# Kernel tuning notes

Hardware: AMD Instinct MI355X
Metric: run time of the kernel (lower is better)

## Reference

```python
import jax, jax.numpy as jnp
import numpy as np

B, C, N = 8, 512, 2048
C8 = C // 8


def setup_inputs() -> dict:
    key = jax.random.key(0)
    kx, kq, kk, kv, kg = jax.random.split(key, 5)
    return {
        "x": jax.random.normal(kx, (B, C, N), dtype=jnp.float32),
        "Wq": jax.random.normal(kq, (C8, C), dtype=jnp.float32) * (1.0 / np.sqrt(C)),
        "Wk": jax.random.normal(kk, (C8, C), dtype=jnp.float32) * (1.0 / np.sqrt(C)),
        "Wv": jax.random.normal(kv, (C, C), dtype=jnp.float32) * (1.0 / np.sqrt(C)),
        # torch init is gamma=0.0; use a small random value so the attention
        # branch contributes to the output.
        "gamma": jax.random.uniform(kg, (1,), dtype=jnp.float32),
    }


def reference(x, Wq, Wk, Wv, gamma):
    # 1x1 convs == per-position linear maps over channels
    f = jnp.einsum("oc,bcn->bon", Wq, x)   # [B, C/8, N]
    g = jnp.einsum("oc,bcn->bon", Wk, x)   # [B, C/8, N]
    h = jnp.einsum("oc,bcn->bon", Wv, x)   # [B, C,   N]
    # scores[b,n,m] = sum_c f[b,c,n] * g[b,c,m]  (unscaled, as in source)
    scores = jnp.einsum("bcn,bcm->bnm", f, g)  # [B, N, N]
    # softmax over dim=1 (the query-position axis) — atypical but faithful
    beta = jax.nn.softmax(scores, axis=1)
    # o = gamma * h @ beta + x
    o = gamma[0] * jnp.einsum("bcn,bnm->bcm", h, beta) + x
    return o
```

## Files before the change

kernel.cpp:

```cpp
#include <hip/hip_runtime.h>
#include <hip/hip_bf16.h>
#include <math.h>

#define NB 8
#define NC 512
#define NN 2048

typedef unsigned short u16;
typedef __attribute__((ext_vector_type(8))) short short8;
typedef __attribute__((ext_vector_type(4))) float f32x4;

__device__ __forceinline__ float bf16_to_f32(u16 v) {
  union { unsigned int u; float f; } c; c.u = ((unsigned int)v) << 16; return c.f;
}
__device__ __forceinline__ u16 f32_to_bf16(float f) {
  __hip_bfloat16 h = __float2bfloat16(f);
  union { __hip_bfloat16 h; u16 u; } c; c.h = h; return c.u;
}
__device__ __forceinline__ void split2(float v, unsigned short& hi, unsigned short& lo) {
  hi = f32_to_bf16(v);
  lo = f32_to_bf16(v - bf16_to_f32(hi));
}

__device__ __forceinline__ void gl_lds16(const void* g, void* l) {
  __builtin_amdgcn_global_load_lds(
      (const __attribute__((address_space(1))) unsigned int*)g,
      (__attribute__((address_space(3))) unsigned int*)l, 16, 0, 0);
}

__device__ __forceinline__ void stage128x32(const u16* __restrict__ src, size_t row_base,
                                            int selems, int k0, u16* lds, int tid) {
#pragma unroll
  for (int s = 0; s < 2; ++s) {
    int flat = s * 4096 + tid * 16;
    int row = flat >> 6;
    int kb  = flat & 63;
    const char* g = (const char*)(src + (row_base + row) * (size_t)selems + k0) + kb;
    u16* l = lds + s * 2048 + (tid & ~63) * 8;
    gl_lds16(g, l);
  }
}

__global__ __launch_bounds__(256)
void xsplit_kernel(const float* __restrict__ x,
                   const float* __restrict__ Wq, const float* __restrict__ Wk,
                   const float* __restrict__ Wv,
                   u16* __restrict__ xThi, u16* __restrict__ xTlo,
                   u16* __restrict__ Whi, u16* __restrict__ Wlo) {
  const int b = blockIdx.z, c0 = blockIdx.y * 64, n0 = blockIdx.x * 64;
  const int tid = threadIdx.x;

  int fid = blockIdx.x + 32 * (blockIdx.y + 8 * blockIdx.z);
  if (fid < 320) {
    int idx = (fid * 256 + tid) * 4;
    int r = idx >> 9, c = idx & 511;
    const float* src;
    if (r < 64)       src = Wq + (size_t)r * NC + c;
    else if (r < 128) src = Wk + (size_t)(r - 64) * NC + c;
    else              src = Wv + (size_t)(r - 128) * NC + c;
    float4 v = *(const float4*)src;
    ushort4 hi, lo;
    split2(v.x, hi.x, lo.x); split2(v.y, hi.y, lo.y);
    split2(v.z, hi.z, lo.z); split2(v.w, hi.w, lo.w);
    *(ushort4*)&Whi[idx] = hi;
    *(ushort4*)&Wlo[idx] = lo;
  }

  __shared__ float t[64][65];
  const int tx = tid & 15, ty = tid >> 4;
#pragma unroll
  for (int r = 0; r < 4; ++r) {
    int c = r * 16 + ty;
    float4 v = *(const float4*)&x[((size_t)b * NC + c0 + c) * NN + n0 + tx * 4];
    t[c][tx * 4 + 0] = v.x; t[c][tx * 4 + 1] = v.y;
    t[c][tx * 4 + 2] = v.z; t[c][tx * 4 + 3] = v.w;
  }
  __syncthreads();
#pragma unroll
  for (int r = 0; r < 4; ++r) {
    int n = r * 16 + ty;
    ushort4 hi, lo;
    split2(t[tx * 4 + 0][n], hi.x, lo.x);
    split2(t[tx * 4 + 1][n], hi.y, lo.y);
    split2(t[tx * 4 + 2][n], hi.z, lo.z);
    split2(t[tx * 4 + 3][n], hi.w, lo.w);
    size_t off = ((size_t)b * NN + n0 + n) * NC + c0 + tx * 4;
    *(ushort4*)&xThi[off] = hi;
    *(ushort4*)&xTlo[off] = lo;
  }
}

__global__ __launch_bounds__(256)
void proj_mfma_kernel(const u16* __restrict__ xThi, const u16* __restrict__ xTlo,
                      const u16* __restrict__ Whi, const u16* __restrict__ Wlo,
                      u16* __restrict__ fgThi, u16* __restrict__ fgTlo,
                      u16* __restrict__ hw) {
  const int b  = blockIdx.z;
  const int n0 = blockIdx.x * 128;
  const int r0 = blockIdx.y * 128;
  const bool fg = (r0 == 0);

  __shared__ u16 Wh[2][128 * 32], Wl[2][128 * 32], Xh[2][128 * 32], Xl[2][128 * 32];

  const int tid = threadIdx.x, wave = tid >> 6, lane = tid & 63;
  const int quad = lane >> 4, l16 = lane & 15;
  const int wa = (wave >> 1) * 64, wb = (wave & 1) * 64;
  const size_t xrow = (size_t)b * NN + n0;

  f32x4 acc[4][4];
#pragma unroll
  for (int i = 0; i < 4; ++i)
#pragma unroll
    for (int j = 0; j < 4; ++j) acc[i][j] = (f32x4){0.f, 0.f, 0.f, 0.f};

  stage128x32(Whi, r0, NC, 0, Wh[0], tid);
  stage128x32(xThi, xrow, NC, 0, Xh[0], tid);
  if (fg) {
    stage128x32(Wlo, r0, NC, 0, Wl[0], tid);
    stage128x32(xTlo, xrow, NC, 0, Xl[0], tid);
  }

  const int KIT = NC / 32;
  for (int ki = 0; ki < KIT; ++ki) {
    __syncthreads();
    if (ki + 1 < KIT) {
      const int nb = (ki + 1) & 1, k1 = (ki + 1) * 32;
      stage128x32(Whi, r0, NC, k1, Wh[nb], tid);
      stage128x32(xThi, xrow, NC, k1, Xh[nb], tid);
      if (fg) {
        stage128x32(Wlo, r0, NC, k1, Wl[nb], tid);
        stage128x32(xTlo, xrow, NC, k1, Xl[nb], tid);
      }
    }
    const int cur = ki & 1;

    if (fg) {
      short8 ah[4], al[4], bh[4], bl[4];
#pragma unroll
      for (int i = 0; i < 4; ++i) {
        ah[i] = *(short8*)&Wh[cur][(wa + i * 16 + l16) * 32 + quad * 8];
        al[i] = *(short8*)&Wl[cur][(wa + i * 16 + l16) * 32 + quad * 8];
      }
#pragma unroll
      for (int j = 0; j < 4; ++j) {
        bh[j] = *(short8*)&Xh[cur][(wb + j * 16 + l16) * 32 + quad * 8];
        bl[j] = *(short8*)&Xl[cur][(wb + j * 16 + l16) * 32 + quad * 8];
      }
#pragma unroll
      for (int i = 0; i < 4; ++i)
#pragma unroll
        for (int j = 0; j < 4; ++j) {
          acc[i][j] = __builtin_amdgcn_mfma_f32_16x16x32_bf16(ah[i], bh[j], acc[i][j], 0, 0, 0);
          acc[i][j] = __builtin_amdgcn_mfma_f32_16x16x32_bf16(ah[i], bl[j], acc[i][j], 0, 0, 0);
          acc[i][j] = __builtin_amdgcn_mfma_f32_16x16x32_bf16(al[i], bh[j], acc[i][j], 0, 0, 0);
        }
    } else {
      short8 ah[4], bh[4];
#pragma unroll
      for (int i = 0; i < 4; ++i)
        ah[i] = *(short8*)&Xh[cur][(wa + i * 16 + l16) * 32 + quad * 8];
#pragma unroll
      for (int j = 0; j < 4; ++j)
        bh[j] = *(short8*)&Wh[cur][(wb + j * 16 + l16) * 32 + quad * 8];
#pragma unroll
      for (int i = 0; i < 4; ++i)
#pragma unroll
        for (int j = 0; j < 4; ++j)
          acc[i][j] = __builtin_amdgcn_mfma_f32_16x16x32_bf16(ah[i], bh[j], acc[i][j], 0, 0, 0);
    }
  }

  if (fg) {
#pragma unroll
    for (int i = 0; i < 4; ++i)
#pragma unroll
      for (int j = 0; j < 4; ++j) {
        int rb = wa + i * 16 + quad * 4;
        int n  = n0 + wb + j * 16 + l16;
        ushort4 hi, lo;
        split2(acc[i][j][0], hi.x, lo.x); split2(acc[i][j][1], hi.y, lo.y);
        split2(acc[i][j][2], hi.z, lo.z); split2(acc[i][j][3], hi.w, lo.w);
        size_t off = ((size_t)b * NN + n) * 128 + rb;
        *(ushort4*)&fgThi[off] = hi;
        *(ushort4*)&fgTlo[off] = lo;
      }
  } else {
#pragma unroll
    for (int i = 0; i < 4; ++i)
#pragma unroll
      for (int j = 0; j < 4; ++j) {
        int nb = n0 + wa + i * 16 + quad * 4;
        int c  = r0 - 128 + wb + j * 16 + l16;
        ushort4 hi;
        hi.x = f32_to_bf16(acc[i][j][0]); hi.y = f32_to_bf16(acc[i][j][1]);
        hi.z = f32_to_bf16(acc[i][j][2]); hi.w = f32_to_bf16(acc[i][j][3]);
        *(ushort4*)&hw[((size_t)b * NC + c) * NN + nb] = hi;
      }
  }
}

__global__ __launch_bounds__(512, 4)
void attn_out_kernel(const u16* __restrict__ fgThi, const u16* __restrict__ fgTlo,
                     const u16* __restrict__ hw, const float* __restrict__ x,
                     const float* __restrict__ gamma, float* __restrict__ out) {
  const int s = blockIdx.x;
  const int xcd = s & 7;
  const int t = s >> 3;
  const int mt = t & 31;
  const int hi6 = t >> 5;
  const int combo = (hi6 << 3) | xcd;
  const int b = combo >> 1;
  const int ch = combo & 1;
  const int m0 = mt * 64;
  const int c0 = ch * 256;

  __shared__ u16 Fh[2][64 * 64], Fl[2][64 * 64];
  __shared__ u16 Hs[256 * 64];
  __shared__ u16 Ps[64 * 64];
  float* Dn = (float*)Ps;

  const int tid = threadIdx.x, wave = tid >> 6, lane = tid & 63;
  const int quad = lane >> 4, l16 = lane & 15;
  const int ws_n = (wave >> 2) * 32, ws_m = (wave & 3) * 16;
  const int wv_c = (wave >> 1) * 64, wv_m = (wave & 1) * 32;

  const size_t frow = (size_t)b * NN;
  const size_t hrow = (size_t)b * NC + c0;

  short8 gh[2], gl[2];
#pragma unroll
  for (int k = 0; k < 2; ++k) {
    size_t o = (frow + m0 + ws_m + l16) * 128 + 64 + k * 32 + quad * 8;
    gh[k] = *(const short8*)&fgThi[o];
    gl[k] = *(const short8*)&fgTlo[o];
  }

  {
    int flat = tid * 16;
    int row = flat >> 7, chunk = (flat >> 4) & 7;
    int kb = ((chunk ^ (row & 7)) << 4);
    gl_lds16((const char*)(fgThi + (frow + row) * 128) + kb, Fh[0] + (tid & ~63) * 8);
    gl_lds16((const char*)(fgTlo + (frow + row) * 128) + kb, Fl[0] + (tid & ~63) * 8);
#pragma unroll
    for (int s2 = 0; s2 < 4; ++s2) {
      int f2 = s2 * 8192 + tid * 16;
      int r2 = f2 >> 7, c2 = (f2 >> 4) & 7;
      gl_lds16((const char*)(hw + (hrow + r2) * NN) + ((c2 ^ (r2 & 7)) << 4),
               Hs + s2 * 4096 + (tid & ~63) * 8);
    }
  }
  __syncthreads();

  float dsum = 0.f;
  f32x4 ao[4][2];
#pragma unroll
  for (int i = 0; i < 4; ++i)
#pragma unroll
    for (int j = 0; j < 2; ++j) ao[i][j] = (f32x4){0.f, 0.f, 0.f, 0.f};

  const int NT = NN / 64;
  for (int it = 0; it < NT; ++it) {
    const int cur = it & 1;

    if (it > 0) {
      const int n1 = it * 64;
#pragma unroll
      for (int s2 = 0; s2 < 4; ++s2) {
        int f2 = s2 * 8192 + tid * 16;
        int r2 = f2 >> 7, c2 = (f2 >> 4) & 7;
        gl_lds16((const char*)(hw + (hrow + r2) * NN + n1) + ((c2 ^ (r2 & 7)) << 4),
                 Hs + s2 * 4096 + (tid & ~63) * 8);
      }
    }
    if (it + 1 < NT) {
      const int n1 = (it + 1) * 64;
      int flat = tid * 16;
      int row = flat >> 7, chunk = (flat >> 4) & 7;
      int kb = ((chunk ^ (row & 7)) << 4);
      gl_lds16((const char*)(fgThi + (frow + n1 + row) * 128) + kb,
               Fh[cur ^ 1] + (tid & ~63) * 8);
      gl_lds16((const char*)(fgTlo + (frow + n1 + row) * 128) + kb,
               Fl[cur ^ 1] + (tid & ~63) * 8);
    }

    f32x4 as[2];
#pragma unroll
    for (int i = 0; i < 2; ++i) as[i] = (f32x4){0.f, 0.f, 0.f, 0.f};
#pragma unroll
    for (int k = 0; k < 2; ++k) {
      short8 fh[2], fl[2];
#pragma unroll
      for (int i = 0; i < 2; ++i) {
        int rr = ws_n + i * 16 + l16;
        int ci = (((k * 4 + quad) ^ (rr & 7)) << 3);
        fh[i] = *(short8*)&Fh[cur][rr * 64 + ci];
        fl[i] = *(short8*)&Fl[cur][rr * 64 + ci];
      }
#pragma unroll
      for (int i = 0; i < 2; ++i) {
        as[i] = __builtin_amdgcn_mfma_f32_16x16x32_bf16(fh[i], gh[k], as[i], 0, 0, 0);
        as[i] = __builtin_amdgcn_mfma_f32_16x16x32_bf16(fh[i], gl[k], as[i], 0, 0, 0);
        as[i] = __builtin_amdgcn_mfma_f32_16x16x32_bf16(fl[i], gh[k], as[i], 0, 0, 0);
      }
    }

    {
      int m = ws_m + l16;
#pragma unroll
      for (int i = 0; i < 2; ++i) {
        float e0 = __expf(as[i][0]);
        float e1 = __expf(as[i][1]);
        float e2 = __expf(as[i][2]);
        float e3 = __expf(as[i][3]);
        dsum += (e0 + e1) + (e2 + e3);
        ushort4 pk;
        pk.x = f32_to_bf16(e0); pk.y = f32_to_bf16(e1);
        pk.z = f32_to_bf16(e2); pk.w = f32_to_bf16(e3);
        int nb = ws_n * 2 + i * 32 + quad * 8;
        int chunk = nb >> 4;
        int off = (nb & 15) >> 1;
        *(ushort4*)&Ps[m * 64 + ((chunk ^ (m & 7)) << 3) + off] = pk;
      }
    }

    if (it + 1 < NT) asm volatile("s_waitcnt vmcnt(2)" ::: "memory");
    else             asm volatile("s_waitcnt vmcnt(0)" ::: "memory");
    asm volatile("s_waitcnt lgkmcnt(0)" ::: "memory");
    __builtin_amdgcn_s_barrier();

#pragma unroll
    for (int k = 0; k < 2; ++k) {
      short8 hh[4], pb[2];
#pragma unroll
      for (int i = 0; i < 4; ++i) {
        int rr = wv_c + i * 16 + l16;
        hh[i] = *(short8*)&Hs[rr * 64 + ((((k * 4 + quad)) ^ (rr & 7)) << 3)];
      }
#pragma unroll
      for (int j = 0; j < 2; ++j) {
        int rm = wv_m + j * 16 + l16;
        pb[j] = *(short8*)&Ps[rm * 64 + ((((k * 4 + quad)) ^ (rm & 7)) << 3)];
      }
#pragma unroll
      for (int i = 0; i < 4; ++i)
#pragma unroll
        for (int j = 0; j < 2; ++j)
          ao[i][j] = __builtin_amdgcn_mfma_f32_16x16x32_bf16(hh[i], pb[j], ao[i][j], 0, 0, 0);
    }

    __syncthreads();
  }

  dsum += __shfl_xor(dsum, 16);
  dsum += __shfl_xor(dsum, 32);
  if (tid < 64) Dn[tid] = 0.f;
  __syncthreads();
  if (quad == 0) atomicAdd(&Dn[ws_m + l16], dsum);
  __syncthreads();

  const float g = gamma[0];
  float invd[2];
#pragma unroll
  for (int j = 0; j < 2; ++j)
    invd[j] = g / Dn[wv_m + j * 16 + l16];

#pragma unroll
  for (int i = 0; i < 4; ++i) {
#pragma unroll
    for (int j = 0; j < 2; ++j) {
      const int c = c0 + wv_c + i * 16 + quad * 4;
      const int m = m0 + wv_m + j * 16 + l16;
#pragma unroll
      for (int r = 0; r < 4; ++r) {
        size_t off = ((size_t)b * NC + c + r) * NN + m;
        out[off] = fmaf(invd[j], ao[i][j][r], x[off]);
      }
    }
  }
}

extern "C" void kernel_launch(void* const* d_in, const int* in_sizes, int n_in,
                              void* d_out, int out_size, void* d_ws, size_t ws_size,
                              hipStream_t stream) {
  const float* x     = (const float*)d_in[0];
  const float* Wq    = (const float*)d_in[1];
  const float* Wk    = (const float*)d_in[2];
  const float* Wv    = (const float*)d_in[3];
  const float* gamma = (const float*)d_in[4];
  float* out = (float*)d_out;

  char* ws = (char*)d_ws;
  u16*   xThi  = (u16*)ws;
  u16*   xTlo  = (u16*)(ws + 16777216);
  u16*   Whi   = (u16*)(ws + 33554432);
  u16*   Wlo   = (u16*)(ws + 34209792);
  u16*   fgThi = (u16*)(ws + 67108864);
  u16*   fgTlo = (u16*)(ws + 71303168);
  u16*   hw    = (u16*)(ws + 75497472);

  xsplit_kernel<<<dim3(NN / 64, NC / 64, NB), 256, 0, stream>>>(
      x, Wq, Wk, Wv, xThi, xTlo, Whi, Wlo);
  proj_mfma_kernel<<<dim3(NN / 128, 5, NB), 256, 0, stream>>>(
      xThi, xTlo, Whi, Wlo, fgThi, fgTlo, hw);
  attn_out_kernel<<<dim3(512), 512, 0, stream>>>(fgThi, fgTlo, hw, x, gamma, out);
}
```

Baseline: 199.2 us.

## Split projection into separate fg and h kernels; raise MFMA wave priority in attention

The combined projection kernel, where one block in five did the three-pass split-bf16 f/g work (a load imbalance), becomes two kernels. proj_fg uses 64-row tiles across two blocks per position tile, so the costly 3-MFMA work is spread over more blocks. proj_h handles the single-pass Wv projection with no divergent branches or unused lo-buffer LDS. In the attention kernel, s_setprio raises wave priority around the MFMA sections to favour matrix issue. The split adds an extra kernel launch and reloads the x tiles for the fg blocks.

```diff
diff --git a/kernel.cpp b/kernel.cpp
--- a/kernel.cpp
+++ b/kernel.cpp
@@ -39,6 +39,15 @@
     u16* l = lds + s * 2048 + (tid & ~63) * 8;
     gl_lds16(g, l);
   }
+}
+
+__device__ __forceinline__ void stage64x32(const u16* __restrict__ src, size_t row_base,
+                                           int selems, int k0, u16* lds, int tid) {
+  int flat = tid * 16;
+  int row = flat >> 6;
+  int kb  = flat & 63;
+  const char* g = (const char*)(src + (row_base + row) * (size_t)selems + k0) + kb;
+  gl_lds16(g, lds + (tid & ~63) * 8);
 }
 
 __global__ __launch_bounds__(256)
@@ -91,16 +100,87 @@
 }
 
 __global__ __launch_bounds__(256)
-void proj_mfma_kernel(const u16* __restrict__ xThi, const u16* __restrict__ xTlo,
-                      const u16* __restrict__ Whi, const u16* __restrict__ Wlo,
-                      u16* __restrict__ fgThi, u16* __restrict__ fgTlo,
-                      u16* __restrict__ hw) {
+void proj_fg_kernel(const u16* __restrict__ xThi, const u16* __restrict__ xTlo,
+                    const u16* __restrict__ Whi, const u16* __restrict__ Wlo,
+                    u16* __restrict__ fgThi, u16* __restrict__ fgTlo) {
   const int b  = blockIdx.z;
   const int n0 = blockIdx.x * 128;
-  const int r0 = blockIdx.y * 128;
-  const bool fg = (r0 == 0);
-
-  __shared__ u16 Wh[2][128 * 32], Wl[2][128 * 32], Xh[2][128 * 32], Xl[2][128 * 32];
+  const int r0 = blockIdx.y * 64;
+
+  __shared__ u16 Wh[2][64 * 32], Wl[2][64 * 32], Xh[2][128 * 32], Xl[2][128 * 32];
+
+  const int tid = threadIdx.x, wave = tid >> 6, lane = tid & 63;
+  const int quad = lane >> 4, l16 = lane & 15;
+  const int wa = (wave >> 1) * 32, wb = (wave & 1) * 64;
+  const size_t xrow = (size_t)b * NN + n0;
+
+  f32x4 acc[2][4];
+#pragma unroll
+  for (int i = 0; i < 2; ++i)
+#pragma unroll
+    for (int j = 0; j < 4; ++j) acc[i][j] = (f32x4){0.f, 0.f, 0.f, 0.f};
+
+  stage64x32(Whi, r0, NC, 0, Wh[0], tid);
+  stage64x32(Wlo, r0, NC, 0, Wl[0], tid);
+  stage128x32(xThi, xrow, NC, 0, Xh[0], tid);
+  stage128x32(xTlo, xrow, NC, 0, Xl[0], tid);
+
+  const int KIT = NC / 32;
+  for (int ki = 0; ki < KIT; ++ki) {
+    __syncthreads();
+    if (ki + 1 < KIT) {
+      const int nb = (ki + 1) & 1, k1 = (ki + 1) * 32;
+      stage64x32(Whi, r0, NC, k1, Wh[nb], tid);
+      stage64x32(Wlo, r0, NC, k1, Wl[nb], tid);
+      stage128x32(xThi, xrow, NC, k1, Xh[nb], tid);
+      stage128x32(xTlo, xrow, NC, k1, Xl[nb], tid);
+    }
+    const int cur = ki & 1;
+
+    short8 ah[2], al[2], bh[4], bl[4];
+#pragma unroll
+    for (int i = 0; i < 2; ++i) {
+      ah[i] = *(short8*)&Wh[cur][(wa + i * 16 + l16) * 32 + quad * 8];
+      al[i] = *(short8*)&Wl[cur][(wa + i * 16 + l16) * 32 + quad * 8];
+    }
+#pragma unroll
+    for (int j = 0; j < 4; ++j) {
+      bh[j] = *(short8*)&Xh[cur][(wb + j * 16 + l16) * 32 + quad * 8];
+      bl[j] = *(short8*)&Xl[cur][(wb + j * 16 + l16) * 32 + quad * 8];
+    }
+#pragma unroll
+    for (int i = 0; i < 2; ++i)
+#pragma unroll
+      for (int j = 0; j < 4; ++j) {
+        acc[i][j] = __builtin_amdgcn_mfma_f32_16x16x32_bf16(ah[i], bh[j], acc[i][j], 0, 0, 0);
+        acc[i][j] = __builtin_amdgcn_mfma_f32_16x16x32_bf16(ah[i], bl[j], acc[i][j], 0, 0, 0);
+        acc[i][j] = __builtin_amdgcn_mfma_f32_16x16x32_bf16(al[i], bh[j], acc[i][j], 0, 0, 0);
+      }
+  }
+
+#pragma unroll
+  for (int i = 0; i < 2; ++i)
+#pragma unroll
+    for (int j = 0; j < 4; ++j) {
+      int rb = r0 + wa + i * 16 + quad * 4;
+      int n  = n0 + wb + j * 16 + l16;
+      ushort4 hi, lo;
+      split2(acc[i][j][0], hi.x, lo.x); split2(acc[i][j][1], hi.y, lo.y);
+      split2(acc[i][j][2], hi.z, lo.z); split2(acc[i][j][3], hi.w, lo.w);
+      size_t off = ((size_t)b * NN + n) * 128 + rb;
+      *(ushort4*)&fgThi[off] = hi;
+      *(ushort4*)&fgTlo[off] = lo;
+    }
+}
+
+__global__ __launch_bounds__(256)
+void proj_h_kernel(const u16* __restrict__ xThi, const u16* __restrict__ Whi,
+                   u16* __restrict__ hw) {
+  const int b  = blockIdx.z;
+  const int n0 = blockIdx.x * 128;
+  const int r0 = 128 + blockIdx.y * 128;
+
+  __shared__ u16 Wh[2][128 * 32], Xh[2][128 * 32];
 
   const int tid = threadIdx.x, wave = tid >> 6, lane = tid & 63;
   const int quad = lane >> 4, l16 = lane & 15;
@@ -115,10 +195,6 @@
 
   stage128x32(Whi, r0, NC, 0, Wh[0], tid);
   stage128x32(xThi, xrow, NC, 0, Xh[0], tid);
-  if (fg) {
-    stage128x32(Wlo, r0, NC, 0, Wl[0], tid);
-    stage128x32(xTlo, xrow, NC, 0, Xl[0], tid);
-  }
 
   const int KIT = NC / 32;
   for (int ki = 0; ki < KIT; ++ki) {
@@ -127,76 +203,34 @@
       const int nb = (ki + 1) & 1, k1 = (ki + 1) * 32;
       stage128x32(Whi, r0, NC, k1, Wh[nb], tid);
       stage128x32(xThi, xrow, NC, k1, Xh[nb], tid);
-      if (fg) {
-        stage128x32(Wlo, r0, NC, k1, Wl[nb], tid);
-        stage128x32(xTlo, xrow, NC, k1, Xl[nb], tid);
-      }
     }
     const int cur = ki & 1;
 
-    if (fg) {
-      short8 ah[4], al[4], bh[4], bl[4];
-#pragma unroll
-      for (int i = 0; i < 4; ++i) {
-        ah[i] = *(short8*)&Wh[cur][(wa + i * 16 + l16) * 32 + quad * 8];
-        al[i] = *(short8*)&Wl[cur][(wa + i * 16 + l16) * 32 + quad * 8];
-      }
-#pragma unroll
-      for (int j = 0; j < 4; ++j) {
-        bh[j] = *(short8*)&Xh[cur][(wb + j * 16 + l16) * 32 + quad * 8];
-        bl[j] = *(short8*)&Xl[cur][(wb + j * 16 + l16) * 32 + quad * 8];
-      }
-#pragma unroll
-      for (int i = 0; i < 4; ++i)
-#pragma unroll
-        for (int j = 0; j < 4; ++j) {
-          acc[i][j] = __builtin_amdgcn_mfma_f32_16x16x32_bf16(ah[i], bh[j], acc[i][j], 0, 0, 0);
-          acc[i][j] = __builtin_amdgcn_mfma_f32_16x16x32_bf16(ah[i], bl[j], acc[i][j], 0, 0, 0);
-          acc[i][j] = __builtin_amdgcn_mfma_f32_16x16x32_bf16(al[i], bh[j], acc[i][j], 0, 0, 0);
-        }
-    } else {
-      short8 ah[4], bh[4];
-#pragma unroll
-      for (int i = 0; i < 4; ++i)
-        ah[i] = *(short8*)&Xh[cur][(wa + i * 16 + l16) * 32 + quad * 8];
+    short8 ah[4], bh[4];
+#pragma unroll
+    for (int i = 0; i < 4; ++i)
+      ah[i] = *(short8*)&Xh[cur][(wa + i * 16 + l16) * 32 + quad * 8];
+#pragma unroll
+    for (int j = 0; j < 4; ++j)
+      bh[j] = *(short8*)&Wh[cur][(wb + j * 16 + l16) * 32 + quad * 8];
+#pragma unroll
+    for (int i = 0; i < 4; ++i)
 #pragma unroll
       for (int j = 0; j < 4; ++j)
-        bh[j] = *(short8*)&Wh[cur][(wb + j * 16 + l16) * 32 + quad * 8];
-#pragma unroll
-      for (int i = 0; i < 4; ++i)
-#pragma unroll
-        for (int j = 0; j < 4; ++j)
-          acc[i][j] = __builtin_amdgcn_mfma_f32_16x16x32_bf16(ah[i], bh[j], acc[i][j], 0, 0, 0);
-    }
-  }
-
-  if (fg) {
-#pragma unroll
-    for (int i = 0; i < 4; ++i)
-#pragma unroll
-      for (int j = 0; j < 4; ++j) {
-        int rb = wa + i * 16 + quad * 4;
-        int n  = n0 + wb + j * 16 + l16;
-        ushort4 hi, lo;
-        split2(acc[i][j][0], hi.x, lo.x); split2(acc[i][j][1], hi.y, lo.y);
-        split2(acc[i][j][2], hi.z, lo.z); split2(acc[i][j][3], hi.w, lo.w);
-        size_t off = ((size_t)b * NN + n) * 128 + rb;
-        *(ushort4*)&fgThi[off] = hi;
-        *(ushort4*)&fgTlo[off] = lo;
-      }
-  } else {
-#pragma unroll
-    for (int i = 0; i < 4; ++i)
-#pragma unroll
-      for (int j = 0; j < 4; ++j) {
-        int nb = n0 + wa + i * 16 + quad * 4;
-        int c  = r0 - 128 + wb + j * 16 + l16;
-        ushort4 hi;
-        hi.x = f32_to_bf16(acc[i][j][0]); hi.y = f32_to_bf16(acc[i][j][1]);
-        hi.z = f32_to_bf16(acc[i][j][2]); hi.w = f32_to_bf16(acc[i][j][3]);
-        *(ushort4*)&hw[((size_t)b * NC + c) * NN + nb] = hi;
-      }
-  }
+        acc[i][j] = __builtin_amdgcn_mfma_f32_16x16x32_bf16(ah[i], bh[j], acc[i][j], 0, 0, 0);
+  }
+
+#pragma unroll
+  for (int i = 0; i < 4; ++i)
+#pragma unroll
+    for (int j = 0; j < 4; ++j) {
+      int nb = n0 + wa + i * 16 + quad * 4;
+      int c  = r0 - 128 + wb + j * 16 + l16;
+      ushort4 hi;
+      hi.x = f32_to_bf16(acc[i][j][0]); hi.y = f32_to_bf16(acc[i][j][1]);
+      hi.z = f32_to_bf16(acc[i][j][2]); hi.w = f32_to_bf16(acc[i][j][3]);
+      *(ushort4*)&hw[((size_t)b * NC + c) * NN + nb] = hi;
+    }
 }
 
 __global__ __launch_bounds__(512, 4)
@@ -286,6 +320,7 @@
     f32x4 as[2];
 #pragma unroll
     for (int i = 0; i < 2; ++i) as[i] = (f32x4){0.f, 0.f, 0.f, 0.f};
+    __builtin_amdgcn_s_setprio(1);
 #pragma unroll
     for (int k = 0; k < 2; ++k) {
       short8 fh[2], fl[2];
@@ -303,6 +338,7 @@
         as[i] = __builtin_amdgcn_mfma_f32_16x16x32_bf16(fl[i], gh[k], as[i], 0, 0, 0);
       }
     }
+    __builtin_amdgcn_s_setprio(0);
 
     {
       int m = ws_m + l16;
@@ -328,6 +364,7 @@
     asm volatile("s_waitcnt lgkmcnt(0)" ::: "memory");
     __builtin_amdgcn_s_barrier();
 
+    __builtin_amdgcn_s_setprio(1);
 #pragma unroll
     for (int k = 0; k < 2; ++k) {
       short8 hh[4], pb[2];
@@ -347,6 +384,7 @@
         for (int j = 0; j < 2; ++j)
           ao[i][j] = __builtin_amdgcn_mfma_f32_16x16x32_bf16(hh[i], pb[j], ao[i][j], 0, 0, 0);
     }
+    __builtin_amdgcn_s_setprio(0);
 
     __syncthreads();
   }
@@ -400,7 +438,8 @@
 
   xsplit_kernel<<<dim3(NN / 64, NC / 64, NB), 256, 0, stream>>>(
       x, Wq, Wk, Wv, xThi, xTlo, Whi, Wlo);
-  proj_mfma_kernel<<<dim3(NN / 128, 5, NB), 256, 0, stream>>>(
-      xThi, xTlo, Whi, Wlo, fgThi, fgTlo, hw);
+  proj_fg_kernel<<<dim3(NN / 128, 2, NB), 256, 0, stream>>>(
+      xThi, xTlo, Whi, Wlo, fgThi, fgTlo);
+  proj_h_kernel<<<dim3(NN / 128, 4, NB), 256, 0, stream>>>(xThi, Whi, hw);
   attn_out_kernel<<<dim3(512), 512, 0, stream>>>(fgThi, fgTlo, hw, x, gamma, out);
 }
```

New measurement: 191.2 us. 4.0% less time.
